# Kernel tuning notes

Hardware: AMD Instinct MI355X
Metric: run time of the kernel (lower is better)

## Reference

```python
import jax, jax.numpy as jnp
import numpy as np

ALPHA = 1.702
EPS_RMS = 1e-6
W_LOAD = 0.01
W_IMP = 0.01
W_AUX = 1.0
LIMIT = 7.0
K_TOP = 4


def swiglu(x, alpha=ALPHA, limit=LIMIT):
    x_glu = jnp.clip(x[..., ::2], -limit, limit)
    x_lin = jnp.clip(x[..., 1::2], -limit, limit)
    return x_glu * jax.nn.sigmoid(x_glu * alpha) + (x_lin + 1.0)


def setup_inputs() -> dict:
    key = jax.random.key(0)
    ks = jax.random.split(key, 4)
    T, H, I, E = 2048, 512, 512, 8
    x = jax.random.normal(ks[0], (T, H), dtype=jnp.float32)
    norm_scale = jnp.ones((H,), jnp.float32)
    gate_w = jax.random.normal(ks[1], (E, H), jnp.float32) * 0.02
    gate_b = jnp.zeros((E,), jnp.float32)
    mlp1_w = jax.random.normal(ks[2], (E, 2 * I, H), jnp.float32) * 0.02
    mlp1_b = jnp.zeros((E, 2 * I), jnp.float32)
    mlp2_w = jax.random.normal(ks[3], (E, H, I), jnp.float32) * 0.02
    mlp2_b = jnp.zeros((E, H), jnp.float32)
    return {"x": x, "norm_scale": norm_scale, "gate_w": gate_w, "gate_b": gate_b,
            "mlp1_w": mlp1_w, "mlp1_b": mlp1_b, "mlp2_w": mlp2_w, "mlp2_b": mlp2_b}


def reference(x, norm_scale, gate_w, gate_b, mlp1_w, mlp1_b, mlp2_w, mlp2_b):
    T, H = x.shape
    E = gate_w.shape[0]
    K = K_TOP
    # RMSNorm (fp32 math as in torch module)
    t = x * jax.lax.rsqrt(jnp.mean(x * x, axis=-1, keepdims=True) + EPS_RMS) * norm_scale
    # gating
    gate_logits = t @ gate_w.T + gate_b                      # [T, E]
    gate_probs = jax.nn.softmax(gate_logits, axis=-1)
    expert_weights, experts_indices = jax.lax.top_k(gate_probs, K)
    expert_weights = expert_weights / expert_weights.sum(axis=-1, keepdims=True)
    # per-token per-expert combine coefficient (sum of slot weights routed to e)
    coeff = jnp.zeros((T, E), x.dtype).at[jnp.arange(T)[:, None], experts_indices].add(expert_weights)
    # dense expert compute (math-equivalent to the gathered einsums; avoids
    # materializing per-token weight matrices)
    h = jnp.einsum('th,ech->tec', t, mlp1_w) + mlp1_b[None]  # [T, E, 2I]
    a = swiglu(h)                                            # [T, E, I]
    y = jnp.einsum('tei,ehi->teh', a, mlp2_w) + mlp2_b[None] # [T, E, H]
    out = jnp.einsum('teh,te->th', y, coeff) + x
    # aux losses (replicates the torch code exactly, incl. D-doubling quirk)
    P = gate_probs.mean(axis=0)                              # [E]
    counts = jax.vmap(lambda col: jnp.zeros((E,), x.dtype).at[col].add(1.0), in_axes=1)(experts_indices)  # [K, E]
    doubling = (2.0 ** (K - jnp.arange(K))).astype(x.dtype)  # D_i = 2*(D_{i-1}+c_i)
    D = (doubling[:, None] * counts).sum(axis=0) / (T * K)
    loss_load = W_LOAD * E * (P * D).sum()
    importance = gate_logits.sum(axis=0)
    cv = jnp.std(importance, ddof=1) / (importance.mean() + 1e-6)
    loss_imp = W_IMP * cv ** 2
    aux_loss = W_AUX * (loss_load + loss_imp)
    return out, aux_loss
```

## Files before the change

kernel.cpp:

```cpp
#include <hip/hip_runtime.h>
#include <stdint.h>

#define ALPHA 1.702f
#define LIMIT 7.0f

typedef float f32x4 __attribute__((ext_vector_type(4)));
typedef __bf16 bf16x8 __attribute__((ext_vector_type(8)));

static __device__ __forceinline__ unsigned short f2bf(float f) {
    union { float f; uint32_t u; } v; v.f = f;
    uint32_t u = v.u;
    return (unsigned short)((u + 0x7FFFu + ((u >> 16) & 1u)) >> 16);
}

#define GLL16(GP, LP) __builtin_amdgcn_global_load_lds( \
    (const __attribute__((address_space(1))) void*)(GP), \
    (__attribute__((address_space(3))) void*)(LP), 16, 0, 0)

__global__ __launch_bounds__(256) void prep_kernel(
    const float* __restrict__ w1, const float* __restrict__ w2,
    unsigned short* __restrict__ w1p, unsigned short* __restrict__ w2b,
    const float* __restrict__ x,
    const float* __restrict__ norm_scale,
    const float* __restrict__ gate_w,
    const float* __restrict__ gate_b,
    const float* __restrict__ b2,
    unsigned short* __restrict__ t_bf,
    float* __restrict__ coeff,
    float* __restrict__ accum,
    float* __restrict__ out)
{
    __shared__ float red[4][48];
    if (blockIdx.x < 6144) {
        const int idx = blockIdx.x * 256 + threadIdx.x;
        const int n1 = 1048576;
        if (idx < n1) {
            const int e = idx >> 17;
            const int rem = idx & 131071;
            const int r = rem >> 7;
            const int c = rem & 127;
            const int src = (r < 512) ? (2 * r) : (2 * (r - 512) + 1);
            float4 v = ((const float4*)w1)[(e << 17) + (src << 7) + c];
            ushort4 o = { f2bf(v.x), f2bf(v.y), f2bf(v.z), f2bf(v.w) };
            ((ushort4*)w1p)[idx] = o;
        } else {
            const int i2 = idx - n1;
            float4 v = ((const float4*)w2)[i2];
            ushort4 o = { f2bf(v.x), f2bf(v.y), f2bf(v.z), f2bf(v.w) };
            ((ushort4*)w2b)[i2] = o;
        }
        return;
    }
    const int bid = blockIdx.x - 6144;
    const int wave = threadIdx.x >> 6;
    const int lane = threadIdx.x & 63;

    float accP[8], accI[8], accC[32];
    #pragma unroll
    for (int e = 0; e < 8; ++e) { accP[e] = 0.f; accI[e] = 0.f; }
    #pragma unroll
    for (int i = 0; i < 32; ++i) accC[i] = 0.f;

    #pragma unroll
    for (int it = 0; it < 2; ++it) {
        const int t = bid * 8 + wave * 2 + it;
        const float4* xr = (const float4*)(x + t * 512);
        float4 x0 = xr[lane * 2];
        float4 x1 = xr[lane * 2 + 1];
        float ss = x0.x*x0.x + x0.y*x0.y + x0.z*x0.z + x0.w*x0.w
                 + x1.x*x1.x + x1.y*x1.y + x1.z*x1.z + x1.w*x1.w;
        #pragma unroll
        for (int off = 32; off > 0; off >>= 1) ss += __shfl_xor(ss, off, 64);
        const float rstd = rsqrtf(ss * (1.f / 512.f) + 1e-6f);
        const float4* sr = (const float4*)norm_scale;
        float4 s0 = sr[lane * 2], s1 = sr[lane * 2 + 1];
        float tv[8];
        tv[0] = x0.x * rstd * s0.x; tv[1] = x0.y * rstd * s0.y;
        tv[2] = x0.z * rstd * s0.z; tv[3] = x0.w * rstd * s0.w;
        tv[4] = x1.x * rstd * s1.x; tv[5] = x1.y * rstd * s1.y;
        tv[6] = x1.z * rstd * s1.z; tv[7] = x1.w * rstd * s1.w;
        uint32_t p0 = (uint32_t)f2bf(tv[0]) | ((uint32_t)f2bf(tv[1]) << 16);
        uint32_t p1 = (uint32_t)f2bf(tv[2]) | ((uint32_t)f2bf(tv[3]) << 16);
        uint32_t p2 = (uint32_t)f2bf(tv[4]) | ((uint32_t)f2bf(tv[5]) << 16);
        uint32_t p3 = (uint32_t)f2bf(tv[6]) | ((uint32_t)f2bf(tv[7]) << 16);
        uint4 pk; pk.x = p0; pk.y = p1; pk.z = p2; pk.w = p3;
        ((uint4*)(t_bf + t * 512))[lane] = pk;
        float le[8];
        #pragma unroll
        for (int e = 0; e < 8; ++e) {
            const float4* gw = (const float4*)(gate_w + e * 512);
            float4 g0 = gw[lane * 2], g1 = gw[lane * 2 + 1];
            float d = tv[0]*g0.x + tv[1]*g0.y + tv[2]*g0.z + tv[3]*g0.w
                    + tv[4]*g1.x + tv[5]*g1.y + tv[6]*g1.z + tv[7]*g1.w;
            #pragma unroll
            for (int off = 32; off > 0; off >>= 1) d += __shfl_xor(d, off, 64);
            le[e] = d + gate_b[e];
        }
        float mx = le[0];
        #pragma unroll
        for (int e = 1; e < 8; ++e) mx = fmaxf(mx, le[e]);
        float pe[8], se = 0.f;
        #pragma unroll
        for (int e = 0; e < 8; ++e) { pe[e] = __expf(le[e] - mx); se += pe[e]; }
        const float sinv = 1.f / se;
        #pragma unroll
        for (int e = 0; e < 8; ++e) pe[e] *= sinv;
        unsigned picked = 0;
        int ik[4]; float wk[4];
        #pragma unroll
        for (int k = 0; k < 4; ++k) {
            float bv = -1.f; int bi = 0;
            #pragma unroll
            for (int e = 0; e < 8; ++e)
                if (!(picked & (1u << e)) && pe[e] > bv) { bv = pe[e]; bi = e; }
            ik[k] = bi; wk[k] = bv; picked |= (1u << bi);
        }
        const float winv = 1.f / (wk[0] + wk[1] + wk[2] + wk[3]);
        float nw[4];
        #pragma unroll
        for (int k = 0; k < 4; ++k) nw[k] = wk[k] * winv;
        float ce[8];
        #pragma unroll
        for (int e = 0; e < 8; ++e) {
            float c = 0.f;
            #pragma unroll
            for (int k = 0; k < 4; ++k) c += (ik[k] == e) ? nw[k] : 0.f;
            ce[e] = c;
        }
        if (lane == 0) {
            #pragma unroll
            for (int e = 0; e < 8; ++e) coeff[t * 8 + e] = ce[e];
        }
        #pragma unroll
        for (int e = 0; e < 8; ++e) { accP[e] += pe[e]; accI[e] += le[e]; }
        #pragma unroll
        for (int k = 0; k < 4; ++k)
            #pragma unroll
            for (int e = 0; e < 8; ++e)
                accC[k * 8 + e] += (ik[k] == e) ? 1.f : 0.f;
        float ov[8];
        ov[0] = x0.x; ov[1] = x0.y; ov[2] = x0.z; ov[3] = x0.w;
        ov[4] = x1.x; ov[5] = x1.y; ov[6] = x1.z; ov[7] = x1.w;
        #pragma unroll
        for (int e = 0; e < 8; ++e) {
            const float4* br = (const float4*)(b2 + e * 512);
            float4 b0 = br[lane * 2], bb1 = br[lane * 2 + 1];
            ov[0] += ce[e] * b0.x; ov[1] += ce[e] * b0.y;
            ov[2] += ce[e] * b0.z; ov[3] += ce[e] * b0.w;
            ov[4] += ce[e] * bb1.x; ov[5] += ce[e] * bb1.y;
            ov[6] += ce[e] * bb1.z; ov[7] += ce[e] * bb1.w;
        }
        float4 o0, o1;
        o0.x = ov[0]; o0.y = ov[1]; o0.z = ov[2]; o0.w = ov[3];
        o1.x = ov[4]; o1.y = ov[5]; o1.z = ov[6]; o1.w = ov[7];
        float4* orow = (float4*)(out + t * 512);
        orow[lane * 2] = o0; orow[lane * 2 + 1] = o1;
    }
    if (lane == 0) {
        #pragma unroll
        for (int e = 0; e < 8; ++e) { red[wave][e] = accP[e]; red[wave][8 + e] = accI[e]; }
        #pragma unroll
        for (int i = 0; i < 32; ++i) red[wave][16 + i] = accC[i];
    }
    __syncthreads();
    if (threadIdx.x < 48) {
        float s = red[0][threadIdx.x] + red[1][threadIdx.x]
                + red[2][threadIdx.x] + red[3][threadIdx.x];
        atomicAdd(accum + threadIdx.x, s);
    }
}

__global__ void aux_kernel(const float* __restrict__ accum, float* __restrict__ aux_out)
{
    if (threadIdx.x == 0 && blockIdx.x == 0) {
        float imp[8];
        float sl = 0.f;
        #pragma unroll
        for (int e = 0; e < 8; ++e) {
            float P = accum[e] * (1.f / 2048.f);
            imp[e] = accum[8 + e];
            float D = (16.f * accum[16 + e] + 8.f * accum[24 + e]
                     + 4.f * accum[32 + e] + 2.f * accum[40 + e]) * (1.f / 8192.f);
            sl += P * D;
        }
        float loss_load = 0.01f * 8.f * sl;
        float mean = 0.f;
        #pragma unroll
        for (int e = 0; e < 8; ++e) mean += imp[e];
        mean *= 0.125f;
        float var = 0.f;
        #pragma unroll
        for (int e = 0; e < 8; ++e) { float d = imp[e] - mean; var += d * d; }
        var *= (1.f / 7.f);
        float cv = sqrtf(var) / (mean + 1e-6f);
        *aux_out = loss_load + 0.01f * cv * cv;
    }
}

__global__ __launch_bounds__(256, 2) void gemm1_swiglu(
    const unsigned short* __restrict__ A,
    const unsigned short* __restrict__ w1p,
    const float* __restrict__ b1,
    const float* __restrict__ coeff,
    unsigned short* __restrict__ As)
{
    __shared__ unsigned short tA[128 * 32];
    __shared__ unsigned short tBg[128 * 32];
    __shared__ unsigned short tBl[128 * 32];
    const int tid = threadIdx.x;
    const int bx = blockIdx.x;
    const int tile_p = bx & 31, tile_m = bx >> 5;
    const int e = tile_p >> 2;
    const int np = (tile_p & 3) * 128;
    const int m0 = tile_m * 128;
    const int lane = tid & 63, wave = tid >> 6;
    const int wm = (wave & 1) * 64, wn = (wave >> 1) * 64;
    const int quad = lane >> 4, l16 = lane & 15;

    f32x4 accG[4][4], accL[4][4];
    #pragma unroll
    for (int i = 0; i < 4; ++i)
        #pragma unroll
        for (int j = 0; j < 4; ++j) {
            f32x4 z = {0.f, 0.f, 0.f, 0.f};
            accG[i][j] = z; accL[i][j] = z;
        }

    const int j0 = tid, j1 = tid + 256;
    const int ar0 = j0 >> 2, ak0 = (j0 & 3) * 8;
    const int ar1 = j1 >> 2, ak1 = (j1 & 3) * 8;

    const unsigned short* Bg = w1p + (e * 1024 + np) * 512;
    const unsigned short* Bl = Bg + 512 * 512;

    for (int k0 = 0; k0 < 512; k0 += 32) {
        GLL16(A + (m0 + ar0) * 512 + k0 + ak0, tA + j0 * 8);
        GLL16(A + (m0 + ar1) * 512 + k0 + ak1, tA + j1 * 8);
        GLL16(Bg + ar0 * 512 + k0 + ak0, tBg + j0 * 8);
        GLL16(Bg + ar1 * 512 + k0 + ak1, tBg + j1 * 8);
        GLL16(Bl + ar0 * 512 + k0 + ak0, tBl + j0 * 8);
        GLL16(Bl + ar1 * 512 + k0 + ak1, tBl + j1 * 8);
        __syncthreads();
        bf16x8 af[4], bg[4], bl[4];
        #pragma unroll
        for (int i = 0; i < 4; ++i) {
            af[i] = *(const bf16x8*)(tA  + (wm + i * 16 + l16) * 32 + quad * 8);
            bg[i] = *(const bf16x8*)(tBg + (wn + i * 16 + l16) * 32 + quad * 8);
            bl[i] = *(const bf16x8*)(tBl + (wn + i * 16 + l16) * 32 + quad * 8);
        }
        #pragma unroll
        for (int i = 0; i < 4; ++i)
            #pragma unroll
            for (int j = 0; j < 4; ++j) {
                accG[i][j] = __builtin_amdgcn_mfma_f32_16x16x32_bf16(af[i], bg[j], accG[i][j], 0, 0, 0);
                accL[i][j] = __builtin_amdgcn_mfma_f32_16x16x32_bf16(af[i], bl[j], accL[i][j], 0, 0, 0);
            }
        __syncthreads();
    }

    float cw[4][4];
    #pragma unroll
    for (int i = 0; i < 4; ++i) {
        const int rowb = m0 + wm + i * 16 + quad * 4;
        #pragma unroll
        for (int r = 0; r < 4; ++r) cw[i][r] = coeff[(rowb + r) * 8 + e];
    }
    #pragma unroll
    for (int j = 0; j < 4; ++j) {
        const int colp = np + wn + j * 16 + l16;
        const float bgv = b1[e * 1024 + 2 * colp];
        const float blv = b1[e * 1024 + 2 * colp + 1];
        #pragma unroll
        for (int i = 0; i < 4; ++i) {
            const int rowb = m0 + wm + i * 16 + quad * 4;
            #pragma unroll
            for (int r = 0; r < 4; ++r) {
                float g = fminf(fmaxf(accG[i][j][r] + bgv, -LIMIT), LIMIT);
                float l = fminf(fmaxf(accL[i][j][r] + blv, -LIMIT), LIMIT);
                float a = g / (1.f + __expf(-ALPHA * g)) + l + 1.f;
                a *= cw[i][r];
                As[(rowb + r) * 4096 + e * 512 + colp] = f2bf(a);
            }
        }
    }
}

__global__ __launch_bounds__(256) void gemm2(
    const unsigned short* __restrict__ As,
    const unsigned short* __restrict__ w2,
    float* __restrict__ out)
{
    __shared__ unsigned short tA[128 * 32];
    __shared__ unsigned short tB[128 * 32];
    const int tid = threadIdx.x;
    const int bx = blockIdx.x;
    const int tile_n = bx & 3;
    const int tile_m = (bx >> 2) & 15;
    const int e = bx >> 6;
    const int m0 = tile_m * 128, n0 = tile_n * 128;
    const int lane = tid & 63, wave = tid >> 6;
    const int wm = (wave & 1) * 64, wn = (wave >> 1) * 64;
    const int quad = lane >> 4, l16 = lane & 15;

    f32x4 acc[4][4];
    #pragma unroll
    for (int i = 0; i < 4; ++i)
        #pragma unroll
        for (int j = 0; j < 4; ++j) { f32x4 z = {0.f, 0.f, 0.f, 0.f}; acc[i][j] = z; }

    const int j0 = tid, j1 = tid + 256;
    const int ar0 = j0 >> 2, ak0 = (j0 & 3) * 8;
    const int ar1 = j1 >> 2, ak1 = (j1 & 3) * 8;

    const unsigned short* Asl = As + e * 512;
    const unsigned short* Bb  = w2 + e * 262144;

    for (int kt = 0; kt < 16; ++kt) {
        const int k0 = kt * 32;
        GLL16(Asl + (m0 + ar0) * 4096 + k0 + ak0, tA + j0 * 8);
        GLL16(Asl + (m0 + ar1) * 4096 + k0 + ak1, tA + j1 * 8);
        GLL16(Bb + (n0 + ar0) * 512 + k0 + ak0, tB + j0 * 8);
        GLL16(Bb + (n0 + ar1) * 512 + k0 + ak1, tB + j1 * 8);
        __syncthreads();
        bf16x8 af[4], bfr[4];
        #pragma unroll
        for (int i = 0; i < 4; ++i) {
            af[i]  = *(const bf16x8*)(tA + (wm + i * 16 + l16) * 32 + quad * 8);
            bfr[i] = *(const bf16x8*)(tB + (wn + i * 16 + l16) * 32 + quad * 8);
        }
        #pragma unroll
        for (int i = 0; i < 4; ++i)
            #pragma unroll
            for (int j = 0; j < 4; ++j)
                acc[i][j] = __builtin_amdgcn_mfma_f32_16x16x32_bf16(af[i], bfr[j], acc[i][j], 0, 0, 0);
        __syncthreads();
    }

    #pragma unroll
    for (int j = 0; j < 4; ++j) {
        const int col = n0 + wn + j * 16 + l16;
        #pragma unroll
        for (int i = 0; i < 4; ++i) {
            const int rowb = m0 + wm + i * 16 + quad * 4;
            #pragma unroll
            for (int r = 0; r < 4; ++r)
                atomicAdd(&out[(rowb + r) * 512 + col], acc[i][j][r]);
        }
    }
}

extern "C" void kernel_launch(void* const* d_in, const int* in_sizes, int n_in,
                              void* d_out, int out_size, void* d_ws, size_t ws_size,
                              hipStream_t stream)
{
    (void)in_sizes; (void)n_in; (void)out_size; (void)ws_size;
    const float* x          = (const float*)d_in[0];
    const float* norm_scale = (const float*)d_in[1];
    const float* gate_w     = (const float*)d_in[2];
    const float* gate_b     = (const float*)d_in[3];
    const float* mlp1_w     = (const float*)d_in[4];
    const float* mlp1_b     = (const float*)d_in[5];
    const float* mlp2_w     = (const float*)d_in[6];
    const float* mlp2_b     = (const float*)d_in[7];
    float* out = (float*)d_out;

    char* ws = (char*)d_ws;
    unsigned short* w1p   = (unsigned short*)(ws);
    unsigned short* w2b   = (unsigned short*)(ws + 8388608);
    unsigned short* tbf   = (unsigned short*)(ws + 12582912);
    unsigned short* As    = (unsigned short*)(ws + 14680064);
    float*          coeff = (float*)(ws + 31457280);
    float*          accum = (float*)(ws + 31522816);

    hipMemsetAsync(accum, 0, 48 * sizeof(float), stream);
    prep_kernel<<<6400, 256, 0, stream>>>(mlp1_w, mlp2_w, w1p, w2b,
                                          x, norm_scale, gate_w, gate_b, mlp2_b,
                                          tbf, coeff, accum, out);
    aux_kernel<<<1, 64, 0, stream>>>(accum, out + 2048 * 512);
    gemm1_swiglu<<<512, 256, 0, stream>>>(tbf, w1p, mlp1_b, coeff, As);
    gemm2<<<512, 256, 0, stream>>>(As, w2b, out);
}
```

Measured before the change: 168.3 us.

## Route tokens sparsely to experts instead of dense all-expert GEMMs

```diff
diff --git a/kernel.cpp b/kernel.cpp
--- a/kernel.cpp
+++ b/kernel.cpp
@@ -12,10 +12,27 @@
     uint32_t u = v.u;
     return (unsigned short)((u + 0x7FFFu + ((u >> 16) & 1u)) >> 16);
 }
+static __device__ __forceinline__ int imin(int a, int b) { return a < b ? a : b; }
 
 #define GLL16(GP, LP) __builtin_amdgcn_global_load_lds( \
     (const __attribute__((address_space(1))) void*)(GP), \
     (__attribute__((address_space(3))) void*)(LP), 16, 0, 0)
+
+static __device__ __forceinline__ int lsw(int row, int kc) {
+    return row * 4 + (kc ^ ((row >> 1) & 3));
+}
+
+static __device__ __forceinline__ bool decode_tile(const int* __restrict__ cnt,
+                                                   int w, int& e, int& tm, int& tn) {
+    int cum = 0;
+    #pragma unroll
+    for (int ee = 0; ee < 8; ++ee) {
+        const int nt = ((cnt[ee] + 63) >> 6) * 4;
+        if (w < cum + nt) { const int loc = w - cum; e = ee; tm = loc >> 2; tn = loc & 3; return true; }
+        cum += nt;
+    }
+    return false;
+}
 
 __global__ __launch_bounds__(256) void prep_kernel(
     const float* __restrict__ w1, const float* __restrict__ w2,
@@ -26,32 +43,40 @@
     const float* __restrict__ gate_b,
     const float* __restrict__ b2,
     unsigned short* __restrict__ t_bf,
-    float* __restrict__ coeff,
+    int* __restrict__ idx,
+    float* __restrict__ wcoef,
     float* __restrict__ accum,
+    int* __restrict__ cnt,
     float* __restrict__ out)
 {
     __shared__ float red[4][48];
-    if (blockIdx.x < 6144) {
-        const int idx = blockIdx.x * 256 + threadIdx.x;
+    __shared__ int   ltok[8][16];
+    __shared__ float lwt[8][16];
+    __shared__ int   lcnt[8];
+    __shared__ int   gbase[8];
+
+    if (blockIdx.x >= 128) {
+        const int i4 = (blockIdx.x - 128) * 256 + threadIdx.x;
         const int n1 = 1048576;
-        if (idx < n1) {
-            const int e = idx >> 17;
-            const int rem = idx & 131071;
+        if (i4 < n1) {
+            const int e = i4 >> 17;
+            const int rem = i4 & 131071;
             const int r = rem >> 7;
             const int c = rem & 127;
             const int src = (r < 512) ? (2 * r) : (2 * (r - 512) + 1);
             float4 v = ((const float4*)w1)[(e << 17) + (src << 7) + c];
             ushort4 o = { f2bf(v.x), f2bf(v.y), f2bf(v.z), f2bf(v.w) };
-            ((ushort4*)w1p)[idx] = o;
+            ((ushort4*)w1p)[i4] = o;
         } else {
-            const int i2 = idx - n1;
+            const int i2 = i4 - n1;
             float4 v = ((const float4*)w2)[i2];
             ushort4 o = { f2bf(v.x), f2bf(v.y), f2bf(v.z), f2bf(v.w) };
             ((ushort4*)w2b)[i2] = o;
         }
         return;
     }
-    const int bid = blockIdx.x - 6144;
+    if (threadIdx.x < 8) lcnt[threadIdx.x] = 0;
+    __syncthreads();
     const int wave = threadIdx.x >> 6;
     const int lane = threadIdx.x & 63;
 
@@ -62,8 +87,8 @@
     for (int i = 0; i < 32; ++i) accC[i] = 0.f;
 
     #pragma unroll
-    for (int it = 0; it < 2; ++it) {
-        const int t = bid * 8 + wave * 2 + it;
+    for (int it = 0; it < 4; ++it) {
+        const int t = blockIdx.x * 16 + wave * 4 + it;
         const float4* xr = (const float4*)(x + t * 512);
         float4 x0 = xr[lane * 2];
         float4 x1 = xr[lane * 2 + 1];
@@ -129,7 +154,11 @@
         }
         if (lane == 0) {
             #pragma unroll
-            for (int e = 0; e < 8; ++e) coeff[t * 8 + e] = ce[e];
+            for (int k = 0; k < 4; ++k) {
+                const int e = ik[k];
+                const int pos = atomicAdd(&lcnt[e], 1);
+                ltok[e][pos] = t; lwt[e][pos] = nw[k];
+            }
         }
         #pragma unroll
         for (int e = 0; e < 8; ++e) { accP[e] += pe[e]; accI[e] += le[e]; }
@@ -163,6 +192,17 @@
         for (int i = 0; i < 32; ++i) red[wave][16 + i] = accC[i];
     }
     __syncthreads();
+    if (threadIdx.x < 8)
+        gbase[threadIdx.x] = atomicAdd(&cnt[threadIdx.x], lcnt[threadIdx.x]);
+    __syncthreads();
+    if (threadIdx.x < 128) {
+        const int e = threadIdx.x >> 4, i = threadIdx.x & 15;
+        if (i < lcnt[e]) {
+            const int g = gbase[e] + i;
+            idx[e * 2048 + g] = ltok[e][i];
+            wcoef[e * 2048 + g] = lwt[e][i];
+        }
+    }
     if (threadIdx.x < 48) {
         float s = red[0][threadIdx.x] + red[1][threadIdx.x]
                 + red[2][threadIdx.x] + red[3][threadIdx.x];
@@ -170,116 +210,121 @@
     }
 }
 
-__global__ void aux_kernel(const float* __restrict__ accum, float* __restrict__ aux_out)
-{
-    if (threadIdx.x == 0 && blockIdx.x == 0) {
-        float imp[8];
-        float sl = 0.f;
-        #pragma unroll
-        for (int e = 0; e < 8; ++e) {
-            float P = accum[e] * (1.f / 2048.f);
-            imp[e] = accum[8 + e];
-            float D = (16.f * accum[16 + e] + 8.f * accum[24 + e]
-                     + 4.f * accum[32 + e] + 2.f * accum[40 + e]) * (1.f / 8192.f);
-            sl += P * D;
-        }
-        float loss_load = 0.01f * 8.f * sl;
-        float mean = 0.f;
-        #pragma unroll
-        for (int e = 0; e < 8; ++e) mean += imp[e];
-        mean *= 0.125f;
-        float var = 0.f;
-        #pragma unroll
-        for (int e = 0; e < 8; ++e) { float d = imp[e] - mean; var += d * d; }
-        var *= (1.f / 7.f);
-        float cv = sqrtf(var) / (mean + 1e-6f);
-        *aux_out = loss_load + 0.01f * cv * cv;
-    }
-}
-
-__global__ __launch_bounds__(256, 2) void gemm1_swiglu(
+__global__ __launch_bounds__(256) void gemm1_swiglu(
     const unsigned short* __restrict__ A,
     const unsigned short* __restrict__ w1p,
     const float* __restrict__ b1,
-    const float* __restrict__ coeff,
-    unsigned short* __restrict__ As)
+    const int* __restrict__ idx,
+    const float* __restrict__ wcoef,
+    const int* __restrict__ cnt,
+    int* __restrict__ tick,
+    unsigned short* __restrict__ As,
+    const float* __restrict__ accum,
+    float* __restrict__ aux_out)
 {
-    __shared__ unsigned short tA[128 * 32];
+    if (blockIdx.x == 512) {
+        if (threadIdx.x == 0) {
+            float imp[8];
+            float sl = 0.f;
+            #pragma unroll
+            for (int e = 0; e < 8; ++e) {
+                float P = accum[e] * (1.f / 2048.f);
+                imp[e] = accum[8 + e];
+                float D = (16.f * accum[16 + e] + 8.f * accum[24 + e]
+                         + 4.f * accum[32 + e] + 2.f * accum[40 + e]) * (1.f / 8192.f);
+                sl += P * D;
+            }
+            float loss_load = 0.01f * 8.f * sl;
+            float mean = 0.f;
+            #pragma unroll
+            for (int e = 0; e < 8; ++e) mean += imp[e];
+            mean *= 0.125f;
+            float var = 0.f;
+            #pragma unroll
+            for (int e = 0; e < 8; ++e) { float d = imp[e] - mean; var += d * d; }
+            var *= (1.f / 7.f);
+            float cv = sqrtf(var) / (mean + 1e-6f);
+            *aux_out = loss_load + 0.01f * cv * cv;
+        }
+        return;
+    }
+    __shared__ unsigned short tA[64 * 32];
     __shared__ unsigned short tBg[128 * 32];
     __shared__ unsigned short tBl[128 * 32];
+    __shared__ int s_w;
     const int tid = threadIdx.x;
-    const int bx = blockIdx.x;
-    const int tile_p = bx & 31, tile_m = bx >> 5;
-    const int e = tile_p >> 2;
-    const int np = (tile_p & 3) * 128;
-    const int m0 = tile_m * 128;
     const int lane = tid & 63, wave = tid >> 6;
-    const int wm = (wave & 1) * 64, wn = (wave >> 1) * 64;
     const int quad = lane >> 4, l16 = lane & 15;
-
-    f32x4 accG[4][4], accL[4][4];
-    #pragma unroll
-    for (int i = 0; i < 4; ++i)
-        #pragma unroll
-        for (int j = 0; j < 4; ++j) {
-            f32x4 z = {0.f, 0.f, 0.f, 0.f};
-            accG[i][j] = z; accL[i][j] = z;
-        }
-
-    const int j0 = tid, j1 = tid + 256;
-    const int ar0 = j0 >> 2, ak0 = (j0 & 3) * 8;
-    const int ar1 = j1 >> 2, ak1 = (j1 & 3) * 8;
-
-    const unsigned short* Bg = w1p + (e * 1024 + np) * 512;
-    const unsigned short* Bl = Bg + 512 * 512;
-
-    for (int k0 = 0; k0 < 512; k0 += 32) {
-        GLL16(A + (m0 + ar0) * 512 + k0 + ak0, tA + j0 * 8);
-        GLL16(A + (m0 + ar1) * 512 + k0 + ak1, tA + j1 * 8);
-        GLL16(Bg + ar0 * 512 + k0 + ak0, tBg + j0 * 8);
-        GLL16(Bg + ar1 * 512 + k0 + ak1, tBg + j1 * 8);
-        GLL16(Bl + ar0 * 512 + k0 + ak0, tBl + j0 * 8);
-        GLL16(Bl + ar1 * 512 + k0 + ak1, tBl + j1 * 8);
+    const int srow = tid >> 2;
+    const int skc  = (tid & 3) ^ ((tid >> 3) & 3);
+    const int soff = skc * 8;
+
+    for (;;) {
+        if (tid == 0) s_w = atomicAdd(tick, 1);
         __syncthreads();
-        bf16x8 af[4], bg[4], bl[4];
-        #pragma unroll
-        for (int i = 0; i < 4; ++i) {
-            af[i] = *(const bf16x8*)(tA  + (wm + i * 16 + l16) * 32 + quad * 8);
-            bg[i] = *(const bf16x8*)(tBg + (wn + i * 16 + l16) * 32 + quad * 8);
-            bl[i] = *(const bf16x8*)(tBl + (wn + i * 16 + l16) * 32 + quad * 8);
-        }
+        const int w = s_w;
+        int e, tm, tn;
+        if (!decode_tile(cnt, w, e, tm, tn)) break;
+        const int cnte = cnt[e];
+        const int m0 = tm * 64, np = tn * 128;
+        const int tok = idx[e * 2048 + imin(m0 + srow, cnte - 1)];
+        const unsigned short* Bg = w1p + (e * 1024 + np) * 512;
+        const unsigned short* Bl = Bg + 512 * 512;
+
+        f32x4 accG[4][2], accL[4][2];
         #pragma unroll
         for (int i = 0; i < 4; ++i)
             #pragma unroll
-            for (int j = 0; j < 4; ++j) {
-                accG[i][j] = __builtin_amdgcn_mfma_f32_16x16x32_bf16(af[i], bg[j], accG[i][j], 0, 0, 0);
-                accL[i][j] = __builtin_amdgcn_mfma_f32_16x16x32_bf16(af[i], bl[j], accL[i][j], 0, 0, 0);
-            }
-        __syncthreads();
-    }
-
-    float cw[4][4];
-    #pragma unroll
-    for (int i = 0; i < 4; ++i) {
-        const int rowb = m0 + wm + i * 16 + quad * 4;
-        #pragma unroll
-        for (int r = 0; r < 4; ++r) cw[i][r] = coeff[(rowb + r) * 8 + e];
-    }
-    #pragma unroll
-    for (int j = 0; j < 4; ++j) {
-        const int colp = np + wn + j * 16 + l16;
-        const float bgv = b1[e * 1024 + 2 * colp];
-        const float blv = b1[e * 1024 + 2 * colp + 1];
-        #pragma unroll
-        for (int i = 0; i < 4; ++i) {
-            const int rowb = m0 + wm + i * 16 + quad * 4;
-            #pragma unroll
-            for (int r = 0; r < 4; ++r) {
-                float g = fminf(fmaxf(accG[i][j][r] + bgv, -LIMIT), LIMIT);
-                float l = fminf(fmaxf(accL[i][j][r] + blv, -LIMIT), LIMIT);
-                float a = g / (1.f + __expf(-ALPHA * g)) + l + 1.f;
-                a *= cw[i][r];
-                As[(rowb + r) * 4096 + e * 512 + colp] = f2bf(a);
+            for (int j = 0; j < 2; ++j) {
+                f32x4 z = {0.f, 0.f, 0.f, 0.f};
+                accG[i][j] = z; accL[i][j] = z;
+            }
+
+        for (int k0 = 0; k0 < 512; k0 += 32) {
+            GLL16(A + tok * 512 + k0 + soff, tA + tid * 8);
+            GLL16(Bg + srow * 512 + k0 + soff,        tBg + tid * 8);
+            GLL16(Bg + (64 + srow) * 512 + k0 + soff, tBg + (tid + 256) * 8);
+            GLL16(Bl + srow * 512 + k0 + soff,        tBl + tid * 8);
+            GLL16(Bl + (64 + srow) * 512 + k0 + soff, tBl + (tid + 256) * 8);
+            __syncthreads();
+            bf16x8 af[4], bg[2], bl[2];
+            #pragma unroll
+            for (int i = 0; i < 4; ++i)
+                af[i] = *(const bf16x8*)(tA + lsw(i * 16 + l16, quad) * 8);
+            #pragma unroll
+            for (int j = 0; j < 2; ++j) {
+                const int c = wave * 32 + j * 16 + l16;
+                bg[j] = *(const bf16x8*)(tBg + lsw(c, quad) * 8);
+                bl[j] = *(const bf16x8*)(tBl + lsw(c, quad) * 8);
+            }
+            #pragma unroll
+            for (int i = 0; i < 4; ++i)
+                #pragma unroll
+                for (int j = 0; j < 2; ++j) {
+                    accG[i][j] = __builtin_amdgcn_mfma_f32_16x16x32_bf16(af[i], bg[j], accG[i][j], 0, 0, 0);
+                    accL[i][j] = __builtin_amdgcn_mfma_f32_16x16x32_bf16(af[i], bl[j], accL[i][j], 0, 0, 0);
+                }
+            __syncthreads();
+        }
+
+        #pragma unroll
+        for (int j = 0; j < 2; ++j) {
+            const int colp = np + wave * 32 + j * 16 + l16;
+            const float bgv = b1[e * 1024 + 2 * colp];
+            const float blv = b1[e * 1024 + 2 * colp + 1];
+            #pragma unroll
+            for (int i = 0; i < 4; ++i) {
+                const int sb = m0 + i * 16 + quad * 4;
+                #pragma unroll
+                for (int r = 0; r < 4; ++r) {
+                    const int s = sb + r;
+                    if (s < cnte) {
+                        float g = fminf(fmaxf(accG[i][j][r] + bgv, -LIMIT), LIMIT);
+                        float l = fminf(fmaxf(accL[i][j][r] + blv, -LIMIT), LIMIT);
+                        float a = g / (1.f + __expf(-ALPHA * g)) + l + 1.f;
+                        As[e * 1048576 + s * 512 + colp] = f2bf(a * wcoef[e * 2048 + s]);
+                    }
+                }
             }
         }
     }
@@ -287,64 +332,74 @@
 
 __global__ __launch_bounds__(256) void gemm2(
     const unsigned short* __restrict__ As,
-    const unsigned short* __restrict__ w2,
+    const unsigned short* __restrict__ w2b,
+    const int* __restrict__ idx,
+    const int* __restrict__ cnt,
+    int* __restrict__ tick,
     float* __restrict__ out)
 {
-    __shared__ unsigned short tA[128 * 32];
+    __shared__ unsigned short tA[64 * 32];
     __shared__ unsigned short tB[128 * 32];
+    __shared__ int s_w;
     const int tid = threadIdx.x;
-    const int bx = blockIdx.x;
-    const int tile_n = bx & 3;
-    const int tile_m = (bx >> 2) & 15;
-    const int e = bx >> 6;
-    const int m0 = tile_m * 128, n0 = tile_n * 128;
     const int lane = tid & 63, wave = tid >> 6;
-    const int wm = (wave & 1) * 64, wn = (wave >> 1) * 64;
     const int quad = lane >> 4, l16 = lane & 15;
-
-    f32x4 acc[4][4];
-    #pragma unroll
-    for (int i = 0; i < 4; ++i)
-        #pragma unroll
-        for (int j = 0; j < 4; ++j) { f32x4 z = {0.f, 0.f, 0.f, 0.f}; acc[i][j] = z; }
-
-    const int j0 = tid, j1 = tid + 256;
-    const int ar0 = j0 >> 2, ak0 = (j0 & 3) * 8;
-    const int ar1 = j1 >> 2, ak1 = (j1 & 3) * 8;
-
-    const unsigned short* Asl = As + e * 512;
-    const unsigned short* Bb  = w2 + e * 262144;
-
-    for (int kt = 0; kt < 16; ++kt) {
-        const int k0 = kt * 32;
-        GLL16(Asl + (m0 + ar0) * 4096 + k0 + ak0, tA + j0 * 8);
-        GLL16(Asl + (m0 + ar1) * 4096 + k0 + ak1, tA + j1 * 8);
-        GLL16(Bb + (n0 + ar0) * 512 + k0 + ak0, tB + j0 * 8);
-        GLL16(Bb + (n0 + ar1) * 512 + k0 + ak1, tB + j1 * 8);
+    const int srow = tid >> 2;
+    const int skc  = (tid & 3) ^ ((tid >> 3) & 3);
+    const int soff = skc * 8;
+
+    for (;;) {
+        if (tid == 0) s_w = atomicAdd(tick, 1);
         __syncthreads();
-        bf16x8 af[4], bfr[4];
+        const int w = s_w;
+        int e, tm, tn;
+        if (!decode_tile(cnt, w, e, tm, tn)) break;
+        const int cnte = cnt[e];
+        const int m0 = tm * 64, n0 = tn * 128;
+        const unsigned short* Asl = As + e * 1048576;
+        const unsigned short* Bb  = w2b + e * 262144;
+
+        f32x4 acc[4][2];
+        #pragma unroll
+        for (int i = 0; i < 4; ++i)
+            #pragma unroll
+            for (int j = 0; j < 2; ++j) { f32x4 z = {0.f, 0.f, 0.f, 0.f}; acc[i][j] = z; }
+
+        for (int k0 = 0; k0 < 512; k0 += 32) {
+            GLL16(Asl + (m0 + srow) * 512 + k0 + soff, tA + tid * 8);
+            GLL16(Bb + (n0 + srow) * 512 + k0 + soff,      tB + tid * 8);
+            GLL16(Bb + (n0 + 64 + srow) * 512 + k0 + soff, tB + (tid + 256) * 8);
+            __syncthreads();
+            bf16x8 af[4], bf[2];
+            #pragma unroll
+            for (int i = 0; i < 4; ++i)
+                af[i] = *(const bf16x8*)(tA + lsw(i * 16 + l16, quad) * 8);
+            #pragma unroll
+            for (int j = 0; j < 2; ++j)
+                bf[j] = *(const bf16x8*)(tB + lsw(wave * 32 + j * 16 + l16, quad) * 8);
+            #pragma unroll
+            for (int i = 0; i < 4; ++i)
+                #pragma unroll
+                for (int j = 0; j < 2; ++j)
+                    acc[i][j] = __builtin_amdgcn_mfma_f32_16x16x32_bf16(af[i], bf[j], acc[i][j], 0, 0, 0);
+            __syncthreads();
+        }
+
         #pragma unroll
         for (int i = 0; i < 4; ++i) {
-            af[i]  = *(const bf16x8*)(tA + (wm + i * 16 + l16) * 32 + quad * 8);
-            bfr[i] = *(const bf16x8*)(tB + (wn + i * 16 + l16) * 32 + quad * 8);
-        }
-        #pragma unroll
-        for (int i = 0; i < 4; ++i)
-            #pragma unroll
-            for (int j = 0; j < 4; ++j)
-                acc[i][j] = __builtin_amdgcn_mfma_f32_16x16x32_bf16(af[i], bfr[j], acc[i][j], 0, 0, 0);
-        __syncthreads();
-    }
-
-    #pragma unroll
-    for (int j = 0; j < 4; ++j) {
-        const int col = n0 + wn + j * 16 + l16;
-        #pragma unroll
-        for (int i = 0; i < 4; ++i) {
-            const int rowb = m0 + wm + i * 16 + quad * 4;
-            #pragma unroll
-            for (int r = 0; r < 4; ++r)
-                atomicAdd(&out[(rowb + r) * 512 + col], acc[i][j][r]);
+            const int sb = m0 + i * 16 + quad * 4;
+            #pragma unroll
+            for (int r = 0; r < 4; ++r) {
+                const int s = sb + r;
+                if (s < cnte) {
+                    const int tok = idx[e * 2048 + s];
+                    #pragma unroll
+                    for (int j = 0; j < 2; ++j) {
+                        const int col = n0 + wave * 32 + j * 16 + l16;
+                        atomicAdd(&out[tok * 512 + col], acc[i][j][r]);
+                    }
+                }
+            }
         }
     }
 }
@@ -369,14 +424,17 @@
     unsigned short* w2b   = (unsigned short*)(ws + 8388608);
     unsigned short* tbf   = (unsigned short*)(ws + 12582912);
     unsigned short* As    = (unsigned short*)(ws + 14680064);
-    float*          coeff = (float*)(ws + 31457280);
-    float*          accum = (float*)(ws + 31522816);
-
-    hipMemsetAsync(accum, 0, 48 * sizeof(float), stream);
-    prep_kernel<<<6400, 256, 0, stream>>>(mlp1_w, mlp2_w, w1p, w2b,
+    int*            idx   = (int*)(ws + 31457280);
+    float*          wcoef = (float*)(ws + 31522816);
+    float*          accum = (float*)(ws + 31588352);
+    int*            cnt   = (int*)(accum + 48);
+    int*            tick  = cnt + 8;
+
+    hipMemsetAsync(accum, 0, 256, stream);
+    prep_kernel<<<6272, 256, 0, stream>>>(mlp1_w, mlp2_w, w1p, w2b,
                                           x, norm_scale, gate_w, gate_b, mlp2_b,
-                                          tbf, coeff, accum, out);
-    aux_kernel<<<1, 64, 0, stream>>>(accum, out + 2048 * 512);
-    gemm1_swiglu<<<512, 256, 0, stream>>>(tbf, w1p, mlp1_b, coeff, As);
-    gemm2<<<512, 256, 0, stream>>>(As, w2b, out);
-}
+                                          tbf, idx, wcoef, accum, cnt, out);
+    gemm1_swiglu<<<513, 256, 0, stream>>>(tbf, w1p, mlp1_b, idx, wcoef, cnt,
+                                          tick, As, accum, out + 2048 * 512);
+    gemm2<<<512, 256, 0, stream>>>(As, w2b, idx, cnt, tick + 1, out);
+}
```

Result: slower. 176.7 us (+5.0%).

## Double-buffer GEMM LDS tiles with swizzle and fold aux kernel into gemm1

Applied to the files above, without the earlier changes.

```diff
diff --git a/kernel.cpp b/kernel.cpp
--- a/kernel.cpp
+++ b/kernel.cpp
@@ -16,6 +16,10 @@
 #define GLL16(GP, LP) __builtin_amdgcn_global_load_lds( \
     (const __attribute__((address_space(1))) void*)(GP), \
     (__attribute__((address_space(3))) void*)(LP), 16, 0, 0)
+
+static __device__ __forceinline__ int lsw(int row, int kc) {
+    return row * 4 + (kc ^ ((row >> 1) & 3));
+}
 
 __global__ __launch_bounds__(256) void prep_kernel(
     const float* __restrict__ w1, const float* __restrict__ w2,
@@ -170,43 +174,43 @@
     }
 }
 
-__global__ void aux_kernel(const float* __restrict__ accum, float* __restrict__ aux_out)
-{
-    if (threadIdx.x == 0 && blockIdx.x == 0) {
-        float imp[8];
-        float sl = 0.f;
-        #pragma unroll
-        for (int e = 0; e < 8; ++e) {
-            float P = accum[e] * (1.f / 2048.f);
-            imp[e] = accum[8 + e];
-            float D = (16.f * accum[16 + e] + 8.f * accum[24 + e]
-                     + 4.f * accum[32 + e] + 2.f * accum[40 + e]) * (1.f / 8192.f);
-            sl += P * D;
-        }
-        float loss_load = 0.01f * 8.f * sl;
-        float mean = 0.f;
-        #pragma unroll
-        for (int e = 0; e < 8; ++e) mean += imp[e];
-        mean *= 0.125f;
-        float var = 0.f;
-        #pragma unroll
-        for (int e = 0; e < 8; ++e) { float d = imp[e] - mean; var += d * d; }
-        var *= (1.f / 7.f);
-        float cv = sqrtf(var) / (mean + 1e-6f);
-        *aux_out = loss_load + 0.01f * cv * cv;
-    }
-}
-
 __global__ __launch_bounds__(256, 2) void gemm1_swiglu(
     const unsigned short* __restrict__ A,
     const unsigned short* __restrict__ w1p,
     const float* __restrict__ b1,
     const float* __restrict__ coeff,
-    unsigned short* __restrict__ As)
+    unsigned short* __restrict__ As,
+    const float* __restrict__ accum,
+    float* __restrict__ aux_out)
 {
-    __shared__ unsigned short tA[128 * 32];
-    __shared__ unsigned short tBg[128 * 32];
-    __shared__ unsigned short tBl[128 * 32];
+    if (blockIdx.x == 512) {
+        if (threadIdx.x == 0) {
+            float imp[8], sl = 0.f;
+            #pragma unroll
+            for (int e = 0; e < 8; ++e) {
+                float P = accum[e] * (1.f / 2048.f);
+                imp[e] = accum[8 + e];
+                float D = (16.f * accum[16 + e] + 8.f * accum[24 + e]
+                         + 4.f * accum[32 + e] + 2.f * accum[40 + e]) * (1.f / 8192.f);
+                sl += P * D;
+            }
+            float loss_load = 0.01f * 8.f * sl;
+            float mean = 0.f;
+            #pragma unroll
+            for (int e = 0; e < 8; ++e) mean += imp[e];
+            mean *= 0.125f;
+            float var = 0.f;
+            #pragma unroll
+            for (int e = 0; e < 8; ++e) { float d = imp[e] - mean; var += d * d; }
+            var *= (1.f / 7.f);
+            float cv = sqrtf(var) / (mean + 1e-6f);
+            *aux_out = loss_load + 0.01f * cv * cv;
+        }
+        return;
+    }
+    __shared__ unsigned short tA[2][4096];
+    __shared__ unsigned short tBg[2][4096];
+    __shared__ unsigned short tBl[2][4096];
     const int tid = threadIdx.x;
     const int bx = blockIdx.x;
     const int tile_p = bx & 31, tile_m = bx >> 5;
@@ -216,6 +220,23 @@
     const int lane = tid & 63, wave = tid >> 6;
     const int wm = (wave & 1) * 64, wn = (wave >> 1) * 64;
     const int quad = lane >> 4, l16 = lane & 15;
+    const int srow = tid >> 2;
+    const int soff = ((tid & 3) ^ ((tid >> 3) & 3)) * 8;
+
+    const unsigned short* Ar0 = A + (m0 + srow) * 512 + soff;
+    const unsigned short* Ar1 = A + (m0 + 64 + srow) * 512 + soff;
+    const unsigned short* Bg = w1p + (e * 1024 + np) * 512;
+    const unsigned short* Bg0 = Bg + srow * 512 + soff;
+    const unsigned short* Bg1 = Bg + (64 + srow) * 512 + soff;
+    const unsigned short* Bl0 = Bg0 + 512 * 512;
+    const unsigned short* Bl1 = Bg1 + 512 * 512;
+
+    int rA[4], rB[4];
+    #pragma unroll
+    for (int i = 0; i < 4; ++i) {
+        rA[i] = lsw(wm + i * 16 + l16, quad) * 8;
+        rB[i] = lsw(wn + i * 16 + l16, quad) * 8;
+    }
 
     f32x4 accG[4][4], accL[4][4];
     #pragma unroll
@@ -226,28 +247,33 @@
             accG[i][j] = z; accL[i][j] = z;
         }
 
-    const int j0 = tid, j1 = tid + 256;
-    const int ar0 = j0 >> 2, ak0 = (j0 & 3) * 8;
-    const int ar1 = j1 >> 2, ak1 = (j1 & 3) * 8;
-
-    const unsigned short* Bg = w1p + (e * 1024 + np) * 512;
-    const unsigned short* Bl = Bg + 512 * 512;
-
-    for (int k0 = 0; k0 < 512; k0 += 32) {
-        GLL16(A + (m0 + ar0) * 512 + k0 + ak0, tA + j0 * 8);
-        GLL16(A + (m0 + ar1) * 512 + k0 + ak1, tA + j1 * 8);
-        GLL16(Bg + ar0 * 512 + k0 + ak0, tBg + j0 * 8);
-        GLL16(Bg + ar1 * 512 + k0 + ak1, tBg + j1 * 8);
-        GLL16(Bl + ar0 * 512 + k0 + ak0, tBl + j0 * 8);
-        GLL16(Bl + ar1 * 512 + k0 + ak1, tBl + j1 * 8);
-        __syncthreads();
+#define STAGE1(s, k0) do { \
+    GLL16(Ar0 + (k0), tA[s] + tid * 8); \
+    GLL16(Ar1 + (k0), tA[s] + (tid + 256) * 8); \
+    GLL16(Bg0 + (k0), tBg[s] + tid * 8); \
+    GLL16(Bg1 + (k0), tBg[s] + (tid + 256) * 8); \
+    GLL16(Bl0 + (k0), tBl[s] + tid * 8); \
+    GLL16(Bl1 + (k0), tBl[s] + (tid + 256) * 8); \
+} while (0)
+
+    STAGE1(0, 0);
+    STAGE1(1, 32);
+    #pragma unroll
+    for (int kt = 0; kt < 16; ++kt) {
+        const int cur = kt & 1;
+        if (kt < 15) asm volatile("s_waitcnt vmcnt(6)" ::: "memory");
+        else         asm volatile("s_waitcnt vmcnt(0)" ::: "memory");
+        asm volatile("s_barrier" ::: "memory");
         bf16x8 af[4], bg[4], bl[4];
         #pragma unroll
         for (int i = 0; i < 4; ++i) {
-            af[i] = *(const bf16x8*)(tA  + (wm + i * 16 + l16) * 32 + quad * 8);
-            bg[i] = *(const bf16x8*)(tBg + (wn + i * 16 + l16) * 32 + quad * 8);
-            bl[i] = *(const bf16x8*)(tBl + (wn + i * 16 + l16) * 32 + quad * 8);
-        }
+            af[i] = *(const bf16x8*)(tA[cur] + rA[i]);
+            bg[i] = *(const bf16x8*)(tBg[cur] + rB[i]);
+            bl[i] = *(const bf16x8*)(tBl[cur] + rB[i]);
+        }
+        asm volatile("s_waitcnt lgkmcnt(0)" ::: "memory");
+        asm volatile("s_barrier" ::: "memory");
+        if (kt < 14) STAGE1(cur, (kt + 2) * 32);
         #pragma unroll
         for (int i = 0; i < 4; ++i)
             #pragma unroll
@@ -255,8 +281,8 @@
                 accG[i][j] = __builtin_amdgcn_mfma_f32_16x16x32_bf16(af[i], bg[j], accG[i][j], 0, 0, 0);
                 accL[i][j] = __builtin_amdgcn_mfma_f32_16x16x32_bf16(af[i], bl[j], accL[i][j], 0, 0, 0);
             }
-        __syncthreads();
-    }
+    }
+#undef STAGE1
 
     float cw[4][4];
     #pragma unroll
@@ -285,13 +311,13 @@
     }
 }
 
-__global__ __launch_bounds__(256) void gemm2(
+__global__ __launch_bounds__(256, 2) void gemm2(
     const unsigned short* __restrict__ As,
-    const unsigned short* __restrict__ w2,
+    const unsigned short* __restrict__ w2b,
     float* __restrict__ out)
 {
-    __shared__ unsigned short tA[128 * 32];
-    __shared__ unsigned short tB[128 * 32];
+    __shared__ unsigned short tA[2][4096];
+    __shared__ unsigned short tB[2][4096];
     const int tid = threadIdx.x;
     const int bx = blockIdx.x;
     const int tile_n = bx & 3;
@@ -301,6 +327,21 @@
     const int lane = tid & 63, wave = tid >> 6;
     const int wm = (wave & 1) * 64, wn = (wave >> 1) * 64;
     const int quad = lane >> 4, l16 = lane & 15;
+    const int srow = tid >> 2;
+    const int soff = ((tid & 3) ^ ((tid >> 3) & 3)) * 8;
+
+    const unsigned short* Ar0 = As + (m0 + srow) * 4096 + e * 512 + soff;
+    const unsigned short* Ar1 = As + (m0 + 64 + srow) * 4096 + e * 512 + soff;
+    const unsigned short* Bb  = w2b + e * 262144;
+    const unsigned short* Br0 = Bb + (n0 + srow) * 512 + soff;
+    const unsigned short* Br1 = Bb + (n0 + 64 + srow) * 512 + soff;
+
+    int rA[4], rB[4];
+    #pragma unroll
+    for (int i = 0; i < 4; ++i) {
+        rA[i] = lsw(wm + i * 16 + l16, quad) * 8;
+        rB[i] = lsw(wn + i * 16 + l16, quad) * 8;
+    }
 
     f32x4 acc[4][4];
     #pragma unroll
@@ -308,33 +349,37 @@
         #pragma unroll
         for (int j = 0; j < 4; ++j) { f32x4 z = {0.f, 0.f, 0.f, 0.f}; acc[i][j] = z; }
 
-    const int j0 = tid, j1 = tid + 256;
-    const int ar0 = j0 >> 2, ak0 = (j0 & 3) * 8;
-    const int ar1 = j1 >> 2, ak1 = (j1 & 3) * 8;
-
-    const unsigned short* Asl = As + e * 512;
-    const unsigned short* Bb  = w2 + e * 262144;
-
+#define STAGE2(s, k0) do { \
+    GLL16(Ar0 + (k0), tA[s] + tid * 8); \
+    GLL16(Ar1 + (k0), tA[s] + (tid + 256) * 8); \
+    GLL16(Br0 + (k0), tB[s] + tid * 8); \
+    GLL16(Br1 + (k0), tB[s] + (tid + 256) * 8); \
+} while (0)
+
+    STAGE2(0, 0);
+    STAGE2(1, 32);
+    #pragma unroll
     for (int kt = 0; kt < 16; ++kt) {
-        const int k0 = kt * 32;
-        GLL16(Asl + (m0 + ar0) * 4096 + k0 + ak0, tA + j0 * 8);
-        GLL16(Asl + (m0 + ar1) * 4096 + k0 + ak1, tA + j1 * 8);
-        GLL16(Bb + (n0 + ar0) * 512 + k0 + ak0, tB + j0 * 8);
-        GLL16(Bb + (n0 + ar1) * 512 + k0 + ak1, tB + j1 * 8);
-        __syncthreads();
-        bf16x8 af[4], bfr[4];
+        const int cur = kt & 1;
+        if (kt < 15) asm volatile("s_waitcnt vmcnt(4)" ::: "memory");
+        else         asm volatile("s_waitcnt vmcnt(0)" ::: "memory");
+        asm volatile("s_barrier" ::: "memory");
+        bf16x8 af[4], bf[4];
         #pragma unroll
         for (int i = 0; i < 4; ++i) {
-            af[i]  = *(const bf16x8*)(tA + (wm + i * 16 + l16) * 32 + quad * 8);
-            bfr[i] = *(const bf16x8*)(tB + (wn + i * 16 + l16) * 32 + quad * 8);
-        }
+            af[i] = *(const bf16x8*)(tA[cur] + rA[i]);
+            bf[i] = *(const bf16x8*)(tB[cur] + rB[i]);
+        }
+        asm volatile("s_waitcnt lgkmcnt(0)" ::: "memory");
+        asm volatile("s_barrier" ::: "memory");
+        if (kt < 14) STAGE2(cur, (kt + 2) * 32);
         #pragma unroll
         for (int i = 0; i < 4; ++i)
             #pragma unroll
             for (int j = 0; j < 4; ++j)
-                acc[i][j] = __builtin_amdgcn_mfma_f32_16x16x32_bf16(af[i], bfr[j], acc[i][j], 0, 0, 0);
-        __syncthreads();
-    }
+                acc[i][j] = __builtin_amdgcn_mfma_f32_16x16x32_bf16(af[i], bf[j], acc[i][j], 0, 0, 0);
+    }
+#undef STAGE2
 
     #pragma unroll
     for (int j = 0; j < 4; ++j) {
@@ -372,11 +417,11 @@
     float*          coeff = (float*)(ws + 31457280);
     float*          accum = (float*)(ws + 31522816);
 
-    hipMemsetAsync(accum, 0, 48 * sizeof(float), stream);
+    hipMemsetAsync(accum, 0, 192, stream);
     prep_kernel<<<6400, 256, 0, stream>>>(mlp1_w, mlp2_w, w1p, w2b,
                                           x, norm_scale, gate_w, gate_b, mlp2_b,
                                           tbf, coeff, accum, out);
-    aux_kernel<<<1, 64, 0, stream>>>(accum, out + 2048 * 512);
-    gemm1_swiglu<<<512, 256, 0, stream>>>(tbf, w1p, mlp1_b, coeff, As);
+    gemm1_swiglu<<<513, 256, 0, stream>>>(tbf, w1p, mlp1_b, coeff, As,
+                                          accum, out + 2048 * 512);
     gemm2<<<512, 256, 0, stream>>>(As, w2b, out);
 }
```

Measured after the change: 166.8 us. About the same (-0.9%).
